# Optimization experiments

Measured on AMD Instinct MI355X. Metric: run time of the kernel, lower is better.

## Reference

```python
import jax, jax.numpy as jnp
import numpy as np

B, S, C, HD = 1, 2048, 2048, 128
H = C // HD  # 16 heads
EPS = float(jnp.finfo(jnp.float32).eps)  # torch nn.RMSNorm default eps


def setup_inputs() -> dict:
    key = jax.random.key(0)
    ks = jax.random.split(key, 10)
    std = 1.0 / np.sqrt(C)
    return {
        "x": jax.random.normal(ks[0], (B, S, C), jnp.float32),
        "rope": jax.random.normal(ks[1], (1, S, 1, HD // 2, 2, 2), jnp.float32),
        "wq": jax.random.normal(ks[2], (C, C), jnp.float32) * std,
        "bq": jax.random.normal(ks[3], (C,), jnp.float32) * 0.01,
        "wk": jax.random.normal(ks[4], (C, C), jnp.float32) * std,
        "bk": jax.random.normal(ks[5], (C,), jnp.float32) * 0.01,
        "wv": jax.random.normal(ks[6], (C, C), jnp.float32) * std,
        "bv": jax.random.normal(ks[7], (C,), jnp.float32) * 0.01,
        "q_norm_w": jnp.ones((HD,), jnp.float32),
        "k_norm_w": jnp.ones((HD,), jnp.float32),
        "wo": jax.random.normal(ks[8], (C, C), jnp.float32) * std,
        "bo": jax.random.normal(ks[9], (C,), jnp.float32) * 0.01,
    }


def _rmsnorm(x, w):
    # x: [..., HD]
    ms = jnp.mean(x * x, axis=-1, keepdims=True)
    return x * jax.lax.rsqrt(ms + EPS) * w


def _apply_rotary(x, rope):
    # x: [B,S,H,HD]; rope: [1,S,1,HD//2,2,2]
    shp = x.shape
    x_ = x.reshape(*shp[:-1], -1, 1, 2)          # [B,S,H,HD/2,1,2]
    out = (rope * x_).sum(axis=-1)               # [B,S,H,HD/2,2]
    return out.reshape(shp)


def reference(x, rope, wq, bq, wk, bk, wv, bv, q_norm_w, k_norm_w, wo, bo):
    q = x @ wq.T + bq
    k = x @ wk.T + bk
    v = x @ wv.T + bv
    q = q.reshape(B, S, H, HD)
    k = k.reshape(B, S, H, HD)
    v = v.reshape(B, S, H, HD)
    q = _rmsnorm(q, q_norm_w)
    k = _rmsnorm(k, k_norm_w)
    q = _apply_rotary(q, rope)
    k = _apply_rotary(k, rope)
    scale = 1.0 / np.sqrt(HD)
    scores = jnp.einsum("bqhd,bkhd->bhqk", q, k) * scale  # [B,H,S,S]
    attn = jax.nn.softmax(scores, axis=-1)
    out = jnp.einsum("bhqk,bkhd->bqhd", attn, v).reshape(B, S, C)
    return out @ wo.T + bo
```

## Files before the change

kernel.cpp:

```cpp
#include <hip/hip_runtime.h>
#include <stdint.h>

#define GLOBAL_AS __attribute__((address_space(1)))
#define LDS_AS    __attribute__((address_space(3)))

typedef unsigned short u16;
typedef __attribute__((ext_vector_type(8))) __bf16 bf16x8;
typedef __attribute__((ext_vector_type(4))) float   f32x4;
typedef __attribute__((ext_vector_type(16))) float  f32x16;
typedef __attribute__((ext_vector_type(2))) float   f32x2;
typedef __attribute__((ext_vector_type(4))) u16     u16x4;

#if __has_builtin(__builtin_amdgcn_exp2f)
#define EXP2(x) __builtin_amdgcn_exp2f(x)
#else
#define EXP2(x) __exp2f(x)
#endif

static __device__ __forceinline__ float bf2f(u16 u) {
    union { uint32_t i; float f; } c; c.i = ((uint32_t)u) << 16; return c.f;
}
static __device__ __forceinline__ u16 f2bf(float f) {
    union { float f; uint32_t i; } c; c.f = f;
    uint32_t r = c.i + 0x7fffu + ((c.i >> 16) & 1u);
    return (u16)(r >> 16);
}
static __device__ __forceinline__ u16 f2bf_fast(float f) {
    union { float f; uint32_t i; } c; c.f = f;
    return (u16)((c.i + 0x8000u) >> 16);
}
static __device__ __forceinline__ void gl_lds16(const void* g, void* l) {
    __builtin_amdgcn_global_load_lds((GLOBAL_AS const uint32_t*)g,
                                     (LDS_AS uint32_t*)l, 16, 0, 0);
}
static __device__ __forceinline__ f32x4 mfma16(bf16x8 a, bf16x8 b, f32x4 c) {
    return __builtin_amdgcn_mfma_f32_16x16x32_bf16(a, b, c, 0, 0, 0);
}
static __device__ __forceinline__ f32x16 mfma32(bf16x8 a, bf16x8 b, f32x16 c) {
    return __builtin_amdgcn_mfma_f32_32x32x16_bf16(a, b, c, 0, 0, 0);
}

__global__ __launch_bounds__(256) void cast5(
    const float* __restrict__ s0, const float* __restrict__ s1,
    const float* __restrict__ s2, const float* __restrict__ s3,
    const float* __restrict__ s4,
    u16* __restrict__ d0, u16* __restrict__ d1, u16* __restrict__ d2,
    u16* __restrict__ d3, u16* __restrict__ d4)
{
    const float* s; u16* d;
    switch (blockIdx.y) {
        case 0: s = s0; d = d0; break;
        case 1: s = s1; d = d1; break;
        case 2: s = s2; d = d2; break;
        case 3: s = s3; d = d3; break;
        default: s = s4; d = d4; break;
    }
    int i = (blockIdx.x * 256 + threadIdx.x) * 8;
    f32x4 v0 = *(const f32x4*)&s[i];
    f32x4 v1 = *(const f32x4*)&s[i + 4];
    u16x4 u0 = { f2bf(v0[0]), f2bf(v0[1]), f2bf(v0[2]), f2bf(v0[3]) };
    u16x4 u1 = { f2bf(v1[0]), f2bf(v1[1]), f2bf(v1[2]), f2bf(v1[3]) };
    *(u16x4*)&d[i] = u0;
    *(u16x4*)&d[i + 4] = u1;
}

__global__ __launch_bounds__(512, 2) void gemm_qkv7(
    const u16* __restrict__ x,
    const u16* __restrict__ wq, const u16* __restrict__ wk, const u16* __restrict__ wv,
    const float* __restrict__ bq, const float* __restrict__ bk, const float* __restrict__ bv,
    u16* __restrict__ q, u16* __restrict__ k, u16* __restrict__ vt)
{
    __shared__ u16 SL[4][16384];
    const int tid = threadIdx.x, l = tid & 63, w = tid >> 6;
    const int wm = w >> 2, wn = w & 3;
    const int lr = l & 15, lg = l >> 4;
    const int lg2 = lg ^ ((lr >> 1) & 3);
    const int bid = blockIdx.x;
    const int j = bid >> 3;
    const int bn = (bid & 7) * 4 + (j & 3);
    const int bm = j >> 2;

    const u16* Ab = x + (size_t)(bm * 256) * 2048;

    const int uA0 = tid,       rA0 = uA0 >> 2, cA0 = (uA0 & 3) ^ ((rA0 >> 1) & 3);
    const int uA1 = 512 + tid, rA1 = uA1 >> 2, cA1 = (uA1 & 3) ^ ((rA1 >> 1) & 3);
    const u16* apA0 = Ab + (size_t)rA0 * 2048 + cA0 * 8;
    const u16* apA1 = Ab + (size_t)rA1 * 2048 + cA1 * 8;
    const int ub0 = tid;
    int ub1 = 512 + tid; if (ub1 > 767) ub1 = 767;
    const int rB0 = ub0 >> 2, cB0 = (ub0 & 3) ^ ((rB0 >> 1) & 3);
    const int rB1 = ub1 >> 2, cB1 = (ub1 & 3) ^ ((rB1 >> 1) & 3);
    const int gr0 = bn * 192 + rB0, gr1 = bn * 192 + rB1;
    const u16* base0 = gr0 < 2048 ? wq : (gr0 < 4096 ? wk : wv);
    const u16* base1 = gr1 < 2048 ? wq : (gr1 < 4096 ? wk : wv);
    const u16* bpB0 = base0 + (size_t)(gr0 & 2047) * 2048 + cB0 * 8;
    const u16* bpB1 = base1 + (size_t)(gr1 & 2047) * 2048 + cB1 * 8;
    const int dA0 = uA0 * 8, dA1 = uA1 * 8;
    const int dB0 = (1024 + tid) * 8, dB1 = (1536 + tid) * 8;

    auto stageA = [&](u16* slot) {
        gl_lds16(apA0, slot + dA0);
        gl_lds16(apA1, slot + dA1);
        apA0 += 32; apA1 += 32;
    };
    auto stageB = [&](u16* slot) {
        gl_lds16(bpB0, slot + dB0);
        gl_lds16(bpB1, slot + dB1);
        bpB0 += 32; bpB1 += 32;
    };

    f32x4 acc[8][3];
#pragma unroll
    for (int mi = 0; mi < 8; ++mi)
#pragma unroll
        for (int nj = 0; nj < 3; ++nj) acc[mi][nj] = (f32x4){0.f, 0.f, 0.f, 0.f};

    stageA((u16*)SL[0]); stageB((u16*)SL[0]);
    stageA((u16*)SL[1]); stageB((u16*)SL[1]);
    stageA((u16*)SL[2]); stageB((u16*)SL[2]);

    const int ar = wm * 128 + lr;
    const int br = wn * 48 + lr;

    auto iter_body = [&](const u16* As0, const u16* As1, u16* sl3, u16* sl4) {
        const u16* Bs0 = As0 + 8192;
        const u16* Bs1 = As1 + 8192;

        asm volatile("s_waitcnt vmcnt(4)" ::: "memory");
        __builtin_amdgcn_s_barrier();
        __builtin_amdgcn_sched_barrier(0);

        bf16x8 b0[3], alo0[4], ahi0[4], b1[3], alo1[4], ahi1[4];

        stageA(sl3);
#pragma unroll
        for (int nj = 0; nj < 3; ++nj)
            b0[nj] = *(const bf16x8*)&Bs0[(br + nj * 16) * 32 + lg2 * 8];
#pragma unroll
        for (int mi = 0; mi < 4; ++mi)
            alo0[mi] = *(const bf16x8*)&As0[(ar + mi * 16) * 32 + lg2 * 8];
#pragma unroll
        for (int mi = 0; mi < 4; ++mi)
            ahi0[mi] = *(const bf16x8*)&As0[(ar + (4 + mi) * 16) * 32 + lg2 * 8];
        __builtin_amdgcn_s_setprio(1);
#pragma unroll
        for (int mi = 0; mi < 4; ++mi)
#pragma unroll
            for (int nj = 0; nj < 3; ++nj)
                acc[mi][nj] = mfma16(alo0[mi], b0[nj], acc[mi][nj]);
        __builtin_amdgcn_s_setprio(0);

        stageB(sl3);
#pragma unroll
        for (int nj = 0; nj < 3; ++nj)
            b1[nj] = *(const bf16x8*)&Bs1[(br + nj * 16) * 32 + lg2 * 8];
#pragma unroll
        for (int mi = 0; mi < 4; ++mi)
            alo1[mi] = *(const bf16x8*)&As1[(ar + mi * 16) * 32 + lg2 * 8];
        __builtin_amdgcn_s_setprio(1);
#pragma unroll
        for (int mi = 0; mi < 4; ++mi)
#pragma unroll
            for (int nj = 0; nj < 3; ++nj)
                acc[4 + mi][nj] = mfma16(ahi0[mi], b0[nj], acc[4 + mi][nj]);
        __builtin_amdgcn_s_setprio(0);

        __builtin_amdgcn_sched_barrier(0);
        __builtin_amdgcn_s_barrier();
        __builtin_amdgcn_sched_barrier(0);

        stageA(sl4);
#pragma unroll
        for (int mi = 0; mi < 4; ++mi)
            ahi1[mi] = *(const bf16x8*)&As1[(ar + (4 + mi) * 16) * 32 + lg2 * 8];
        __builtin_amdgcn_s_setprio(1);
#pragma unroll
        for (int mi = 0; mi < 4; ++mi)
#pragma unroll
            for (int nj = 0; nj < 3; ++nj)
                acc[mi][nj] = mfma16(alo1[mi], b1[nj], acc[mi][nj]);
        __builtin_amdgcn_s_setprio(0);

        stageB(sl4);
        __builtin_amdgcn_s_setprio(1);
#pragma unroll
        for (int mi = 0; mi < 4; ++mi)
#pragma unroll
            for (int nj = 0; nj < 3; ++nj)
                acc[4 + mi][nj] = mfma16(ahi1[mi], b1[nj], acc[4 + mi][nj]);
        __builtin_amdgcn_s_setprio(0);
    };

#pragma unroll 1
    for (int it2 = 0; it2 < 16; ++it2) {
        iter_body((const u16*)SL[0], (const u16*)SL[1], (u16*)SL[3], (u16*)SL[0]);
        iter_body((const u16*)SL[2], (const u16*)SL[3], (u16*)SL[1], (u16*)SL[2]);
    }
    asm volatile("s_waitcnt vmcnt(0)" ::: "memory");

#pragma unroll
    for (int mi = 0; mi < 8; ++mi) {
        int row0 = bm * 256 + wm * 128 + mi * 16 + lg * 4;
#pragma unroll
        for (int nj = 0; nj < 3; ++nj) {
            int col = bn * 192 + wn * 48 + nj * 16 + lr;
            int cs = (col >> 11), cc = col & 2047;
            const float* bp = cs == 0 ? bq : (cs == 1 ? bk : bv);
            float bs = bp[cc];
            if (cs == 2) {
                u16x4 pk = { f2bf(acc[mi][nj][0] + bs), f2bf(acc[mi][nj][1] + bs),
                             f2bf(acc[mi][nj][2] + bs), f2bf(acc[mi][nj][3] + bs) };
                *(u16x4*)&vt[(size_t)cc * 2048 + row0] = pk;
            } else {
                u16* C = cs == 0 ? q : k;
#pragma unroll
                for (int reg = 0; reg < 4; ++reg)
                    C[(size_t)(row0 + reg) * 2048 + cc] = f2bf(acc[mi][nj][reg] + bs);
            }
        }
    }
}

__global__ __launch_bounds__(512, 2) void gemm_out5(
    const u16* __restrict__ a, const u16* __restrict__ wo,
    const float* __restrict__ bo, float* __restrict__ out)
{
    __shared__ u16 SL[4][8192];
    const int tid = threadIdx.x, l = tid & 63, w = tid >> 6;
    const int wm = w >> 2, wn = w & 3;
    const int lr = l & 15, lg = l >> 4;
    const int lg2 = lg ^ ((lr >> 1) & 3);
    const int bid = blockIdx.x;
    const int xcd = bid & 7, j = bid >> 3;
    const int bm = xcd * 2 + (j & 1), bn = j >> 1;

    const u16* Ab = a  + (size_t)(bm * 128) * 2048;
    const u16* Bb = wo + (size_t)(bn * 128) * 2048;

    const int r0 = tid >> 2, c0 = (tid & 3) ^ ((r0 >> 1) & 3);
    const u16* apA = Ab + (size_t)r0 * 2048 + c0 * 8;
    const u16* bpB = Bb + (size_t)r0 * 2048 + c0 * 8;
    const int dA = tid * 8, dB = (512 + tid) * 8;

    auto stage = [&](u16* slot) {
        gl_lds16(apA, slot + dA);
        gl_lds16(bpB, slot + dB);
        apA += 32; bpB += 32;
    };

    f32x4 acc[4][2];
#pragma unroll
    for (int mi = 0; mi < 4; ++mi)
#pragma unroll
        for (int nj = 0; nj < 2; ++nj) acc[mi][nj] = (f32x4){0.f, 0.f, 0.f, 0.f};

    stage((u16*)SL[0]); stage((u16*)SL[1]); stage((u16*)SL[2]);

    auto ob = [&](const u16* As, u16* sln) {
        const u16* Bs = As + 4096;
        asm volatile("s_waitcnt vmcnt(4)" ::: "memory");
        __builtin_amdgcn_s_barrier();
        __builtin_amdgcn_sched_barrier(0);

        stage(sln);

        bf16x8 bf[2], af0[2];
#pragma unroll
        for (int nj = 0; nj < 2; ++nj)
            bf[nj] = *(const bf16x8*)&Bs[(wn * 32 + nj * 16 + lr) * 32 + lg2 * 8];
#pragma unroll
        for (int mi = 0; mi < 2; ++mi)
            af0[mi] = *(const bf16x8*)&As[(wm * 64 + mi * 16 + lr) * 32 + lg2 * 8];
        __builtin_amdgcn_s_setprio(1);
#pragma unroll
        for (int mi = 0; mi < 2; ++mi)
#pragma unroll
            for (int nj = 0; nj < 2; ++nj)
                acc[mi][nj] = mfma16(af0[mi], bf[nj], acc[mi][nj]);
        __builtin_amdgcn_s_setprio(0);
        __builtin_amdgcn_s_barrier();
        __builtin_amdgcn_sched_barrier(0);

        bf16x8 af1[2];
#pragma unroll
        for (int mi = 0; mi < 2; ++mi)
            af1[mi] = *(const bf16x8*)&As[(wm * 64 + (2 + mi) * 16 + lr) * 32 + lg2 * 8];
        __builtin_amdgcn_s_setprio(1);
#pragma unroll
        for (int mi = 0; mi < 2; ++mi)
#pragma unroll
            for (int nj = 0; nj < 2; ++nj)
                acc[2 + mi][nj] = mfma16(af1[mi], bf[nj], acc[2 + mi][nj]);
        __builtin_amdgcn_s_setprio(0);
    };

#pragma unroll 1
    for (int it4 = 0; it4 < 16; ++it4) {
        ob((const u16*)SL[0], (u16*)SL[3]);
        ob((const u16*)SL[1], (u16*)SL[0]);
        ob((const u16*)SL[2], (u16*)SL[1]);
        ob((const u16*)SL[3], (u16*)SL[2]);
    }
    asm volatile("s_waitcnt vmcnt(0)" ::: "memory");

#pragma unroll
    for (int mi = 0; mi < 4; ++mi) {
        int row0 = bm * 128 + wm * 64 + mi * 16 + lg * 4;
#pragma unroll
        for (int nj = 0; nj < 2; ++nj) {
            int col = bn * 128 + wn * 32 + nj * 16 + lr;
            float bs = bo[col];
#pragma unroll
            for (int reg = 0; reg < 4; ++reg)
                out[(size_t)(row0 + reg) * 2048 + col] = acc[mi][nj][reg] + bs;
        }
    }
}

__global__ __launch_bounds__(256) void norm_rope(
    const u16* __restrict__ qb, const u16* __restrict__ kb,
    const float* __restrict__ rope, const float* __restrict__ qw, const float* __restrict__ kw,
    u16* __restrict__ qh, u16* __restrict__ kh)
{
    const int tid = threadIdx.x, l = tid & 63, w = tid >> 6;
    const int rowid = blockIdx.x * 4 + w;
    const int h = rowid & 15, s = rowid >> 4;
    const size_t gbase = (size_t)s * 2048 + h * 128 + 2 * l;

    uint32_t qu = *(const uint32_t*)&qb[gbase];
    uint32_t ku = *(const uint32_t*)&kb[gbase];
    float q0 = bf2f((u16)qu), q1 = bf2f((u16)(qu >> 16));
    float k0 = bf2f((u16)ku), k1 = bf2f((u16)(ku >> 16));

    float sq = q0 * q0 + q1 * q1;
    float sk = k0 * k0 + k1 * k1;
#pragma unroll
    for (int m = 1; m < 64; m <<= 1) {
        sq += __shfl_xor(sq, m);
        sk += __shfl_xor(sk, m);
    }
    const float EPS = 1.1920928955078125e-07f;
    const float SCALE = 0.08838834764831845f * 1.4426950408889634f;
    float rq = rsqrtf(sq * (1.f / 128.f) + EPS) * SCALE;
    float rk = rsqrtf(sk * (1.f / 128.f) + EPS);

    f32x2 wq2 = *(const f32x2*)&qw[2 * l];
    f32x2 wk2 = *(const f32x2*)&kw[2 * l];
    float qn0 = q0 * rq * wq2[0], qn1 = q1 * rq * wq2[1];
    float kn0 = k0 * rk * wk2[0], kn1 = k1 * rk * wk2[1];

    f32x4 rr = *(const f32x4*)&rope[(size_t)s * 256 + l * 4];
    float qo0 = rr[0] * qn0 + rr[1] * qn1;
    float qo1 = rr[2] * qn0 + rr[3] * qn1;
    float ko0 = rr[0] * kn0 + rr[1] * kn1;
    float ko1 = rr[2] * kn0 + rr[3] * kn1;

    const size_t obase = ((size_t)h * 2048 + s) * 128 + 2 * l;
    *(uint32_t*)&qh[obase] = (uint32_t)f2bf(qo0) | ((uint32_t)f2bf(qo1) << 16);
    *(uint32_t*)&kh[obase] = (uint32_t)f2bf(ko0) | ((uint32_t)f2bf(ko1) << 16);
}

__global__ __launch_bounds__(256, 2) void attn(
    const u16* __restrict__ qh, const u16* __restrict__ kh,
    const u16* __restrict__ vt, u16* __restrict__ Opb, float* __restrict__ Lp)
{
    __shared__ u16 Ks[64 * 128];
    __shared__ u16 Vs[128 * 64];
    const int tid = threadIdx.x, l = tid & 63, w = tid >> 6;
    const int h = blockIdx.z, half = blockIdx.y;
    const int q0 = blockIdx.x * 128 + w * 32;
    const int lo = l & 31, hi = l >> 5;
    const float SHIFT = -17.312340490667562f;

    const u16* Kh = kh + (size_t)h * 2048 * 128;
    const u16* Vh = vt + (size_t)h * 128 * 2048;
    const int kvbase = half * 1024;

    bf16x8 qf[8];
#pragma unroll
    for (int i = 0; i < 8; ++i)
        qf[i] = *(const bf16x8*)&qh[((size_t)h * 2048 + q0 + lo) * 128 + i * 16 + hi * 8];

    f32x16 o[4];
#pragma unroll
    for (int dj = 0; dj < 4; ++dj)
#pragma unroll
        for (int r = 0; r < 16; ++r) o[dj][r] = 0.f;
    float lsum = 0.f;

#pragma unroll 1
    for (int t = 0; t < 16; ++t) {
        const int kv0 = kvbase + t * 64;
        __syncthreads();
#pragma unroll
        for (int r = 0; r < 4; ++r) {
            int c = w * 4 + r;
            {
                int row = c * 4 + (l >> 4);
                int u = (l & 15) ^ (row & 7);
                gl_lds16(Kh + (size_t)(kv0 + row) * 128 + u * 8, &Ks[c * 512 + l * 8]);
            }
            {
                int row = c * 8 + (l >> 3);
                int u = (l & 7) ^ (row & 7);
                gl_lds16(Vh + (size_t)row * 2048 + kv0 + u * 8, &Vs[c * 512 + l * 8]);
            }
        }
        __syncthreads();

        f32x16 sc0, sc1;
#pragma unroll
        for (int r = 0; r < 16; ++r) { sc0[r] = SHIFT; sc1[r] = SHIFT; }
        __builtin_amdgcn_s_setprio(1);
#pragma unroll
        for (int i = 0; i < 8; ++i) {
            int u = ((i * 2 + hi) ^ (lo & 7)) * 8;
            bf16x8 kA0 = *(const bf16x8*)&Ks[lo * 128 + u];
            bf16x8 kA1 = *(const bf16x8*)&Ks[(32 + lo) * 128 + u];
            sc0 = mfma32(kA0, qf[i], sc0);
            sc1 = mfma32(kA1, qf[i], sc1);
        }
        __builtin_amdgcn_s_setprio(0);

        uint32_t pa[4][4];
        float ls = 0.f;
#pragma unroll
        for (int c = 0; c < 2; ++c) {
            float pv[16];
#pragma unroll
            for (int r = 0; r < 16; ++r) {
                pv[r] = EXP2(c == 0 ? sc0[r] : sc1[r]);
                ls += pv[r];
            }
#pragma unroll
            for (int s = 0; s < 2; ++s) {
                uint32_t pk0a = (uint32_t)f2bf_fast(pv[(2 * s) * 4 + 0]) |
                                ((uint32_t)f2bf_fast(pv[(2 * s) * 4 + 1]) << 16);
                uint32_t pk0b = (uint32_t)f2bf_fast(pv[(2 * s) * 4 + 2]) |
                                ((uint32_t)f2bf_fast(pv[(2 * s) * 4 + 3]) << 16);
                uint32_t pk1a = (uint32_t)f2bf_fast(pv[(2 * s + 1) * 4 + 0]) |
                                ((uint32_t)f2bf_fast(pv[(2 * s + 1) * 4 + 1]) << 16);
                uint32_t pk1b = (uint32_t)f2bf_fast(pv[(2 * s + 1) * 4 + 2]) |
                                ((uint32_t)f2bf_fast(pv[(2 * s + 1) * 4 + 3]) << 16);
                uint32_t x0a = __shfl_xor(pk0a, 32), x0b = __shfl_xor(pk0b, 32);
                uint32_t x1a = __shfl_xor(pk1a, 32), x1b = __shfl_xor(pk1b, 32);
                int ks = c * 2 + s;
                pa[ks][0] = hi ? x1a : pk0a;
                pa[ks][1] = hi ? x1b : pk0b;
                pa[ks][2] = hi ? pk1a : x0a;
                pa[ks][3] = hi ? pk1b : x0b;
            }
        }
        lsum += ls;

        __builtin_amdgcn_s_setprio(1);
#pragma unroll
        for (int dj = 0; dj < 4; ++dj) {
            int row = dj * 32 + lo;
#pragma unroll
            for (int ks = 0; ks < 4; ++ks) {
                int u = ((ks * 2 + hi) ^ (lo & 7)) * 8;
                bf16x8 vB = *(const bf16x8*)&Vs[row * 64 + u];
                union { uint32_t d[4]; bf16x8 v; } cv;
                cv.d[0] = pa[ks][0]; cv.d[1] = pa[ks][1];
                cv.d[2] = pa[ks][2]; cv.d[3] = pa[ks][3];
                o[dj] = mfma32(cv.v, vB, o[dj]);
            }
        }
        __builtin_amdgcn_s_setprio(0);
    }

    lsum += __shfl_xor(lsum, 32);
    if (hi == 0)
        Lp[(half * 16 + h) * 2048 + q0 + lo] = lsum;
#pragma unroll
    for (int dj = 0; dj < 4; ++dj)
#pragma unroll
        for (int r = 0; r < 16; ++r) {
            int qq = q0 + (r & 3) + 8 * (r >> 2) + 4 * hi;
            Opb[((size_t)(half * 2048) + qq) * 2048 + h * 128 + dj * 32 + lo] =
                f2bf(o[dj][r]);
        }
}

__global__ __launch_bounds__(256) void combine(
    const u16* __restrict__ Opb, const float* __restrict__ Lp, u16* __restrict__ ab)
{
    int idx = (blockIdx.x * 256 + threadIdx.x) * 4;
    int s = idx >> 11, c = idx & 2047, h = c >> 7;
    u16x4 a4 = *(const u16x4*)&Opb[(size_t)s * 2048 + c];
    u16x4 b4 = *(const u16x4*)&Opb[(size_t)(2048 + s) * 2048 + c];
    float rl = 1.0f / (Lp[h * 2048 + s] + Lp[(16 + h) * 2048 + s]);
    u16x4 u = { f2bf((bf2f(a4[0]) + bf2f(b4[0])) * rl),
                f2bf((bf2f(a4[1]) + bf2f(b4[1])) * rl),
                f2bf((bf2f(a4[2]) + bf2f(b4[2])) * rl),
                f2bf((bf2f(a4[3]) + bf2f(b4[3])) * rl) };
    *(u16x4*)&ab[idx] = u;
}

extern "C" void kernel_launch(void* const* d_in, const int* in_sizes, int n_in,
                              void* d_out, int out_size, void* d_ws, size_t ws_size,
                              hipStream_t stream)
{
    (void)in_sizes; (void)n_in; (void)out_size;
    const float* x    = (const float*)d_in[0];
    const float* rope = (const float*)d_in[1];
    const float* wq   = (const float*)d_in[2];
    const float* bq   = (const float*)d_in[3];
    const float* wk   = (const float*)d_in[4];
    const float* bk   = (const float*)d_in[5];
    const float* wv   = (const float*)d_in[6];
    const float* bv   = (const float*)d_in[7];
    const float* qw   = (const float*)d_in[8];
    const float* kw   = (const float*)d_in[9];
    const float* wo   = (const float*)d_in[10];
    const float* bo   = (const float*)d_in[11];
    float* out = (float*)d_out;

    const size_t NE = 2048ull * 2048ull;
    if (ws_size < 13 * NE * 2) return;
    u16* p = (u16*)d_ws;
    u16* xb  = p; p += NE;
    u16* wqb = p; p += NE;
    u16* wkb = p; p += NE;
    u16* wvb = p; p += NE;
    u16* wob = p; p += NE;
    u16* qb  = p; p += NE;
    u16* kb  = p; p += NE;
    u16* vb  = p; p += NE;
    u16* qhb = p; p += NE;
    u16* khb = p; p += NE;
    u16* ab  = p; p += NE;
    u16* vtb = p; p += NE;
    u16* spare = p; p += NE;
    (void)spare; (void)vb;

    u16*   Opb = xb;
    float* Lp  = (float*)qb;

    cast5<<<dim3(2048, 5), 256, 0, stream>>>(x, wq, wk, wv, wo, xb, wqb, wkb, wvb, wob);
    gemm_qkv7<<<256, 512, 0, stream>>>(xb, wqb, wkb, wvb, bq, bk, bv, qb, kb, vtb);
    norm_rope<<<8192, 256, 0, stream>>>(qb, kb, rope, qw, kw, qhb, khb);
    attn<<<dim3(16, 2, 16), 256, 0, stream>>>(qhb, khb, vtb, Opb, Lp);
    combine<<<4096, 256, 0, stream>>>(Opb, Lp, ab);
    gemm_out5<<<256, 512, 0, stream>>>(ab, wob, bo, out);
}
```

Before: 155.4 us.

## Fuse split-KV combine into attention via intra-block LDS reduction

Each attention block now covers 64 queries. Two wave pairs each process one half of the KV range, and their unnormalized outputs and row sums are reduced through shared memory inside the block. This removes the separate combine kernel and the global round trip of partial outputs and log-sums. In exchange, each block allocates a much larger shared buffer, which likely limits residency to one block per CU. Each loaded K/V tile is also now shared by only two waves instead of four.

```diff
diff --git a/kernel.cpp b/kernel.cpp
--- a/kernel.cpp
+++ b/kernel.cpp
@@ -362,19 +362,21 @@
 
 __global__ __launch_bounds__(256, 2) void attn(
     const u16* __restrict__ qh, const u16* __restrict__ kh,
-    const u16* __restrict__ vt, u16* __restrict__ Opb, float* __restrict__ Lp)
+    const u16* __restrict__ vt, u16* __restrict__ ab)
 {
-    __shared__ u16 Ks[64 * 128];
-    __shared__ u16 Vs[128 * 64];
+    __shared__ u16 SB[4][16384];
     const int tid = threadIdx.x, l = tid & 63, w = tid >> 6;
-    const int h = blockIdx.z, half = blockIdx.y;
-    const int q0 = blockIdx.x * 128 + w * 32;
+    const int h = blockIdx.y;
+    const int p = w >> 1;
+    const int q0 = blockIdx.x * 64 + (w & 1) * 32;
     const int lo = l & 31, hi = l >> 5;
     const float SHIFT = -17.312340490667562f;
 
     const u16* Kh = kh + (size_t)h * 2048 * 128;
     const u16* Vh = vt + (size_t)h * 128 * 2048;
-    const int kvbase = half * 1024;
+    const int kvbase = p * 1024;
+    u16* Ks = (u16*)SB[2 * p];
+    u16* Vs = (u16*)SB[2 * p + 1];
 
     bf16x8 qf[8];
 #pragma unroll
@@ -392,18 +394,19 @@
     for (int t = 0; t < 16; ++t) {
         const int kv0 = kvbase + t * 64;
         __syncthreads();
-#pragma unroll
-        for (int r = 0; r < 4; ++r) {
-            int c = w * 4 + r;
-            {
-                int row = c * 4 + (l >> 4);
-                int u = (l & 15) ^ (row & 7);
-                gl_lds16(Kh + (size_t)(kv0 + row) * 128 + u * 8, &Ks[c * 512 + l * 8]);
-            }
-            {
-                int row = c * 8 + (l >> 3);
-                int u = (l & 7) ^ (row & 7);
-                gl_lds16(Vh + (size_t)row * 2048 + kv0 + u * 8, &Vs[c * 512 + l * 8]);
+        if ((w & 1) == 0) {
+#pragma unroll
+            for (int i = 0; i < 16; ++i) {
+                int u = i * 64 + l;
+                int row = u >> 4, cu = (u & 15) ^ (row & 7);
+                gl_lds16(Kh + (size_t)(kv0 + row) * 128 + cu * 8, Ks + u * 8);
+            }
+        } else {
+#pragma unroll
+            for (int i = 0; i < 16; ++i) {
+                int u = i * 64 + l;
+                int row = u >> 3, cu = (u & 7) ^ (row & 7);
+                gl_lds16(Vh + (size_t)row * 2048 + kv0 + cu * 8, Vs + u * 8);
             }
         }
         __syncthreads();
@@ -471,31 +474,35 @@
     }
 
     lsum += __shfl_xor(lsum, 32);
-    if (hi == 0)
-        Lp[(half * 16 + h) * 2048 + q0 + lo] = lsum;
-#pragma unroll
-    for (int dj = 0; dj < 4; ++dj)
-#pragma unroll
-        for (int r = 0; r < 16; ++r) {
-            int qq = q0 + (r & 3) + 8 * (r >> 2) + 4 * hi;
-            Opb[((size_t)(half * 2048) + qq) * 2048 + h * 128 + dj * 32 + lo] =
-                f2bf(o[dj][r]);
-        }
-}
-
-__global__ __launch_bounds__(256) void combine(
-    const u16* __restrict__ Opb, const float* __restrict__ Lp, u16* __restrict__ ab)
-{
-    int idx = (blockIdx.x * 256 + threadIdx.x) * 4;
-    int s = idx >> 11, c = idx & 2047, h = c >> 7;
-    u16x4 a4 = *(const u16x4*)&Opb[(size_t)s * 2048 + c];
-    u16x4 b4 = *(const u16x4*)&Opb[(size_t)(2048 + s) * 2048 + c];
-    float rl = 1.0f / (Lp[h * 2048 + s] + Lp[(16 + h) * 2048 + s]);
-    u16x4 u = { f2bf((bf2f(a4[0]) + bf2f(b4[0])) * rl),
-                f2bf((bf2f(a4[1]) + bf2f(b4[1])) * rl),
-                f2bf((bf2f(a4[2]) + bf2f(b4[2])) * rl),
-                f2bf((bf2f(a4[3]) + bf2f(b4[3])) * rl) };
-    *(u16x4*)&ab[idx] = u;
+
+    __syncthreads();
+    float* sf = (float*)&SB[0][0];
+    if (w >= 2) {
+#pragma unroll
+        for (int dj = 0; dj < 4; ++dj)
+#pragma unroll
+            for (int r = 0; r < 16; ++r) {
+                int qq = (r & 3) + 8 * (r >> 2) + 4 * hi;
+                sf[(w - 2) * 4096 + qq * 128 + dj * 32 + lo] = o[dj][r];
+            }
+        if (hi == 0)
+            sf[8192 + (w - 2) * 32 + lo] = lsum;
+    }
+    __syncthreads();
+    if (w < 2) {
+        float lt = lsum + sf[8192 + w * 32 + lo];
+        float rl = 1.0f / lt;
+#pragma unroll
+        for (int dj = 0; dj < 4; ++dj)
+#pragma unroll
+            for (int r = 0; r < 16; ++r) {
+                int qq = (r & 3) + 8 * (r >> 2) + 4 * hi;
+                float part = sf[w * 4096 + qq * 128 + dj * 32 + lo];
+                float rlq = __shfl(rl, qq);
+                ab[(size_t)(q0 + qq) * 2048 + h * 128 + dj * 32 + lo] =
+                    f2bf((o[dj][r] + part) * rlq);
+            }
+    }
 }
 
 extern "C" void kernel_launch(void* const* d_in, const int* in_sizes, int n_in,
@@ -535,13 +542,9 @@
     u16* spare = p; p += NE;
     (void)spare; (void)vb;
 
-    u16*   Opb = xb;
-    float* Lp  = (float*)qb;
-
     cast5<<<dim3(2048, 5), 256, 0, stream>>>(x, wq, wk, wv, wo, xb, wqb, wkb, wvb, wob);
     gemm_qkv7<<<256, 512, 0, stream>>>(xb, wqb, wkb, wvb, bq, bk, bv, qb, kb, vtb);
     norm_rope<<<8192, 256, 0, stream>>>(qb, kb, rope, qw, kw, qhb, khb);
-    attn<<<dim3(16, 2, 16), 256, 0, stream>>>(qhb, khb, vtb, Opb, Lp);
-    combine<<<4096, 256, 0, stream>>>(Opb, Lp, ab);
+    attn<<<dim3(32, 16), 256, 0, stream>>>(qhb, khb, vtb, ab);
     gemm_out5<<<256, 512, 0, stream>>>(ab, wob, bo, out);
 }
```

After: 184.2 us. 18.6% more time.
